# Optimization experiments

Measured on AMD Instinct MI355X. Metric: run time of the kernel, lower is better.

The kernel has to match this reference:

```python
import jax, jax.numpy as jnp
import numpy as np

B, T, C, H = 4, 2048, 768, 64

def setup_inputs() -> dict:
    key = jax.random.key(0)
    k1, k2, k3, k4 = jax.random.split(key, 4)
    x = jax.random.normal(k1, (B, T, C), dtype=jnp.float32)
    # Dense kernels (glorot-ish scale)
    s = 1.0 / np.sqrt(C)
    Wq = jax.random.normal(k2, (C, H), dtype=jnp.float32) * s
    Wk = jax.random.normal(k3, (C, H), dtype=jnp.float32) * s
    Wv = jax.random.normal(k4, (C, H), dtype=jnp.float32) * s
    return {"x": x, "Wq": Wq, "Wk": Wk, "Wv": Wv}

def reference(x, Wq, Wk, Wv):
    # q, k, v: [B, T, H]
    q = jnp.einsum('btc,ch->bth', x, Wq)
    k = jnp.einsum('btc,ch->bth', x, Wk)
    v = jnp.einsum('btc,ch->bth', x, Wv)
    scale = k.shape[-1] ** -0.5
    # scores: [B, T, T]
    scores = jnp.einsum('bth,bsh->bts', q, k) * scale
    # causal mask: lower-triangular allowed
    causal = jnp.tril(jnp.ones((T, T), dtype=bool))
    scores = jnp.where(causal, scores, -jnp.inf)
    weights = jax.nn.softmax(scores, axis=-1)
    # dropout is inactive at inference (Keras default training=False)
    out = jnp.einsum('bts,bsh->bth', weights, v)
    return out
```

## Files before the change

kernel.cpp:

```cpp
#include <hip/hip_runtime.h>
#include <hip/hip_bf16.h>
#include <math.h>

constexpr int BB = 4;
constexpr int TT = 2048;
constexpr int CC = 768;
constexpr int HH = 64;
constexpr int NSPLIT = 4;

typedef __attribute__((ext_vector_type(8))) short bf16x8;
typedef __attribute__((ext_vector_type(4))) float f32x4;

__device__ inline ushort f2bf(float f) {
    uint u = __float_as_uint(f);
    u += 0x7fffu + ((u >> 16) & 1u);
    return (ushort)(u >> 16);
}

__device__ inline bf16x8 cvt8(const float4 a, const float4 b) {
    union { bf16x8 v; __hip_bfloat162 h[4]; } u;
    u.h[0] = __float22bfloat162_rn(make_float2(a.x, a.y));
    u.h[1] = __float22bfloat162_rn(make_float2(a.z, a.w));
    u.h[2] = __float22bfloat162_rn(make_float2(b.x, b.y));
    u.h[3] = __float22bfloat162_rn(make_float2(b.z, b.w));
    return u.v;
}

__global__ __launch_bounds__(256) void prep_w(const float* __restrict__ Wq,
                                              const float* __restrict__ Wk,
                                              const float* __restrict__ Wv,
                                              ushort* __restrict__ Wt) {
    const int k0  = blockIdx.x * 64;
    const int mat = blockIdx.y;
    const float* W = (mat == 0) ? Wq : (mat == 1) ? Wk : Wv;
    __shared__ ushort tile[64 * 66];
    const int tid = threadIdx.x;

    for (int i = tid; i < 1024; i += 256) {
        int kk = i >> 4, c = i & 15;
        float4 f = ((const float4*)W)[(k0 + kk) * 16 + c];
        ushort* d = &tile[kk * 66 + c * 4];
        d[0] = f2bf(f.x); d[1] = f2bf(f.y); d[2] = f2bf(f.z); d[3] = f2bf(f.w);
    }
    __syncthreads();
    for (int i = tid; i < 512; i += 256) {
        int n = i >> 3, c8 = i & 7;
        bf16x8 v;
        #pragma unroll
        for (int j = 0; j < 8; ++j)
            ((ushort*)&v)[j] = tile[(c8 * 8 + j) * 66 + n];
        *(bf16x8*)&Wt[(size_t)(mat * 64 + n) * CC + k0 + c8 * 8] = v;
    }
}

__global__ __launch_bounds__(256) void qkv_mfma(const float* __restrict__ x,
                                                const ushort* __restrict__ Wt,
                                                ushort* __restrict__ qg,
                                                ushort* __restrict__ kg,
                                                ushort* __restrict__ vtg) {
    __shared__ ushort vts[64 * 24];
    const int tid  = threadIdx.x;
    const int row0 = blockIdx.x * 16;
    const int lane = tid & 63, w = tid >> 6;
    const int l15  = lane & 15, quad = lane >> 4;
    const int cg   = w * 48;

    f32x4 acc[3];
    #pragma unroll
    for (int i = 0; i < 3; ++i) acc[i] = (f32x4){0.f, 0.f, 0.f, 0.f};

    const float* xrow = x + (size_t)(row0 + l15) * CC;
    #pragma unroll 4
    for (int kc = 0; kc < 24; ++kc) {
        const float4* xp = (const float4*)(xrow + kc * 32) + quad * 2;
        bf16x8 a = cvt8(xp[0], xp[1]);
        #pragma unroll
        for (int nt = 0; nt < 3; ++nt) {
            bf16x8 bfr = *(const bf16x8*)
                &Wt[(size_t)(cg + nt * 16 + l15) * CC + kc * 32 + quad * 8];
            acc[nt] = __builtin_amdgcn_mfma_f32_16x16x32_bf16(a, bfr, acc[nt], 0, 0, 0);
        }
    }

    #pragma unroll
    for (int nt = 0; nt < 3; ++nt) {
        int n = cg + nt * 16 + l15;
        #pragma unroll
        for (int r = 0; r < 4; ++r) {
            int row = row0 + quad * 4 + r;
            float vacc = acc[nt][r];
            if (n < 64)       qg[(size_t)row * HH + n] = f2bf(vacc * 0.125f);
            else if (n < 128) kg[(size_t)row * HH + (n - 64)] = f2bf(vacc);
            else              vts[(n - 128) * 24 + (quad * 4 + r)] = f2bf(vacc);
        }
    }
    __syncthreads();
    if (tid < 128) {
        int h = tid >> 1, p = tid & 1;
        int b = row0 >> 11, tl = row0 & 2047;
        bf16x8 v = *(const bf16x8*)&vts[h * 24 + p * 8];
        *(bf16x8*)&vtg[(size_t)b * (HH * TT) + (size_t)h * TT + tl + p * 8] = v;
    }
}

__global__ __launch_bounds__(128) void attn_split(const ushort* __restrict__ qg,
                                                  const ushort* __restrict__ kg,
                                                  const ushort* __restrict__ vtg,
                                                  float* __restrict__ Op,
                                                  float* __restrict__ ml) {
    const int qt2 = blockIdx.x, b = blockIdx.y, split = blockIdx.z;
    const int tid  = threadIdx.x;
    const int lane = tid & 63, w = tid >> 6;
    const int l15  = lane & 15, quad = lane >> 4;
    const int t0   = qt2 * 32;
    const int pidx = ((b * 64 + qt2) << 2) + split;

    const int ntile = (qt2 >> 1) + 1;
    const int lo = (ntile * split) >> 2;
    const int hi = (ntile * (split + 1)) >> 2;

    if (lo >= hi) {
        float4 z = (float4){0.f, 0.f, 0.f, 0.f};
        float4* op4 = (float4*)(Op + (size_t)pidx * 2048);
        #pragma unroll
        for (int j = 0; j < 4; ++j) op4[tid * 4 + j] = z;
        if (tid < 32) {
            ml[pidx * 64 + tid]      = -1e30f;
            ml[pidx * 64 + 32 + tid] = 0.f;
        }
        return;
    }

    __shared__ ushort Ps[2][16 * 72];

    const ushort* qp = &qg[(size_t)(b * TT + t0 + w * 16 + l15) * HH + quad * 8];
    bf16x8 qa0 = *(const bf16x8*)qp;
    bf16x8 qa1 = *(const bf16x8*)(qp + 32);

    f32x4 po[4];
    #pragma unroll
    for (int i = 0; i < 4; ++i) po[i] = (f32x4){0.f, 0.f, 0.f, 0.f};
    float mrun[4] = {-1e30f, -1e30f, -1e30f, -1e30f};
    float lrun[4] = {0.f, 0.f, 0.f, 0.f};

    for (int st = lo; st < hi; ++st) {
        f32x4 sf[4];
        #pragma unroll
        for (int nt = 0; nt < 4; ++nt) {
            const ushort* kp =
                &kg[(size_t)(b * TT + st * 64 + nt * 16 + l15) * HH + quad * 8];
            bf16x8 b0 = *(const bf16x8*)kp;
            bf16x8 b1 = *(const bf16x8*)(kp + 32);
            f32x4 z = (f32x4){0.f, 0.f, 0.f, 0.f};
            z = __builtin_amdgcn_mfma_f32_16x16x32_bf16(qa0, b0, z, 0, 0, 0);
            sf[nt] = __builtin_amdgcn_mfma_f32_16x16x32_bf16(qa1, b1, z, 0, 0, 0);
        }

        float p[4][4];
        float rm[4] = {-1e30f, -1e30f, -1e30f, -1e30f};
        if (st == ntile - 1) {
            #pragma unroll
            for (int nt = 0; nt < 4; ++nt) {
                int s_abs = st * 64 + nt * 16 + l15;
                #pragma unroll
                for (int r = 0; r < 4; ++r) {
                    int t_abs = t0 + w * 16 + quad * 4 + r;
                    float v = (s_abs > t_abs) ? -1e30f : sf[nt][r];
                    p[nt][r] = v;
                    rm[r] = fmaxf(rm[r], v);
                }
            }
        } else {
            #pragma unroll
            for (int nt = 0; nt < 4; ++nt)
                #pragma unroll
                for (int r = 0; r < 4; ++r) {
                    p[nt][r] = sf[nt][r];
                    rm[r] = fmaxf(rm[r], sf[nt][r]);
                }
        }
        float alpha[4], rs[4] = {0.f, 0.f, 0.f, 0.f};
        #pragma unroll
        for (int r = 0; r < 4; ++r) {
            float v = rm[r];
            v = fmaxf(v, __shfl_xor(v, 1, 64));
            v = fmaxf(v, __shfl_xor(v, 2, 64));
            v = fmaxf(v, __shfl_xor(v, 4, 64));
            v = fmaxf(v, __shfl_xor(v, 8, 64));
            float mnew = fmaxf(mrun[r], v);
            alpha[r] = __expf(mrun[r] - mnew);
            mrun[r] = mnew;
        }
        #pragma unroll
        for (int nt = 0; nt < 4; ++nt)
            #pragma unroll
            for (int r = 0; r < 4; ++r) {
                float e = __expf(p[nt][r] - mrun[r]);
                p[nt][r] = e;
                rs[r] += e;
            }
        #pragma unroll
        for (int r = 0; r < 4; ++r) {
            float v = rs[r];
            v += __shfl_xor(v, 1, 64);
            v += __shfl_xor(v, 2, 64);
            v += __shfl_xor(v, 4, 64);
            v += __shfl_xor(v, 8, 64);
            lrun[r] = lrun[r] * alpha[r] + v;
        }
        #pragma unroll
        for (int jj = 0; jj < 4; ++jj)
            #pragma unroll
            for (int r = 0; r < 4; ++r)
                po[jj][r] *= alpha[r];

        #pragma unroll
        for (int nt = 0; nt < 4; ++nt)
            #pragma unroll
            for (int r = 0; r < 4; ++r)
                Ps[w][(quad * 4 + r) * 72 + nt * 16 + l15] = f2bf(p[nt][r]);
        bf16x8 pa0 = *(const bf16x8*)&Ps[w][l15 * 72 + quad * 8];
        bf16x8 pa1 = *(const bf16x8*)&Ps[w][l15 * 72 + 32 + quad * 8];

        #pragma unroll
        for (int jj = 0; jj < 4; ++jj) {
            const ushort* vp =
                &vtg[(size_t)b * (HH * TT) + (size_t)(jj * 16 + l15) * TT + st * 64 + quad * 8];
            bf16x8 b0 = *(const bf16x8*)vp;
            bf16x8 b1 = *(const bf16x8*)(vp + 32);
            po[jj] = __builtin_amdgcn_mfma_f32_16x16x32_bf16(pa0, b0, po[jj], 0, 0, 0);
            po[jj] = __builtin_amdgcn_mfma_f32_16x16x32_bf16(pa1, b1, po[jj], 0, 0, 0);
        }
    }

    #pragma unroll
    for (int jj = 0; jj < 4; ++jj)
        #pragma unroll
        for (int r = 0; r < 4; ++r)
            Op[(size_t)pidx * 2048 + (w * 16 + quad * 4 + r) * 64 + jj * 16 + l15] =
                po[jj][r];
    if (l15 == 0) {
        #pragma unroll
        for (int r = 0; r < 4; ++r) {
            int row = w * 16 + quad * 4 + r;
            ml[pidx * 64 + row]      = mrun[r];
            ml[pidx * 64 + 32 + row] = lrun[r];
        }
    }
}

__global__ __launch_bounds__(256) void attn_merge(const float* __restrict__ Op,
                                                  const float* __restrict__ ml,
                                                  float* __restrict__ out) {
    const int tid = threadIdx.x;
    const int w = tid >> 6, lane = tid & 63;
    const int row = blockIdx.x * 4 + w;
    const int b = row >> 11, t = row & 2047;
    const int qt2 = t >> 5, rl = t & 31;
    const int pbase = ((b * 64 + qt2) << 2);

    float m[NSPLIT], l[NSPLIT];
    #pragma unroll
    for (int i = 0; i < NSPLIT; ++i) {
        m[i] = ml[(pbase + i) * 64 + rl];
        l[i] = ml[(pbase + i) * 64 + 32 + rl];
    }
    float M = fmaxf(fmaxf(m[0], m[1]), fmaxf(m[2], m[3]));
    float wgt[NSPLIT], L = 0.f;
    #pragma unroll
    for (int i = 0; i < NSPLIT; ++i) {
        wgt[i] = __expf(m[i] - M);
        L += wgt[i] * l[i];
    }
    float acc = 0.f;
    #pragma unroll
    for (int i = 0; i < NSPLIT; ++i)
        acc += wgt[i] * Op[(size_t)(pbase + i) * 2048 + rl * 64 + lane];
    out[(size_t)row * HH + lane] = acc / L;
}

extern "C" void kernel_launch(void* const* d_in, const int* in_sizes, int n_in,
                              void* d_out, int out_size, void* d_ws, size_t ws_size,
                              hipStream_t stream)
{
    const float* x  = (const float*)d_in[0];
    const float* Wq = (const float*)d_in[1];
    const float* Wk = (const float*)d_in[2];
    const float* Wv = (const float*)d_in[3];
    float* out = (float*)d_out;

    ushort* qg  = (ushort*)d_ws;
    ushort* kg  = qg  + (size_t)BB * TT * HH;
    ushort* vtg = kg  + (size_t)BB * TT * HH;
    ushort* Wt  = vtg + (size_t)BB * TT * HH;
    float*  Op  = (float*)(Wt + (size_t)3 * HH * CC);
    float*  ml  = Op + (size_t)1024 * 2048;

    prep_w    <<<dim3(12, 3),           dim3(256), 0, stream>>>(Wq, Wk, Wv, Wt);
    qkv_mfma  <<<dim3((BB * TT) / 16),  dim3(256), 0, stream>>>(x, Wt, qg, kg, vtg);
    attn_split<<<dim3(64, BB, NSPLIT),  dim3(128), 0, stream>>>(qg, kg, vtg, Op, ml);
    attn_merge<<<dim3((BB * TT) / 4),   dim3(256), 0, stream>>>(Op, ml, out);
}
```

Before: 139.2 us.

## Prefetch K/V and x/W tiles into registers and raise split count to eight

The QKV projection kernel now keeps a four-deep register ring of x and weight fragments, so global loads are issued ahead of the MFMAs that consume them. The attention split kernel prefetches the next K tile and issues the V loads before the softmax step, hiding load latency behind compute. The KV split count doubles from four to eight, which raises parallelism across the grid. In exchange it doubles the partial-output workspace and merge traffic, launches more empty blocks for short rows, and increases register pressure.

```diff
diff --git a/kernel.cpp b/kernel.cpp
--- a/kernel.cpp
+++ b/kernel.cpp
@@ -6,7 +6,7 @@
 constexpr int TT = 2048;
 constexpr int CC = 768;
 constexpr int HH = 64;
-constexpr int NSPLIT = 4;
+constexpr int NSPLIT = 8;
 
 typedef __attribute__((ext_vector_type(8))) short bf16x8;
 typedef __attribute__((ext_vector_type(4))) float f32x4;
@@ -69,17 +69,38 @@
     #pragma unroll
     for (int i = 0; i < 3; ++i) acc[i] = (f32x4){0.f, 0.f, 0.f, 0.f};
 
-    const float* xrow = x + (size_t)(row0 + l15) * CC;
-    #pragma unroll 4
+    const float*  xrow  = x + (size_t)(row0 + l15) * CC;
+    const ushort* wbase = Wt + (size_t)(cg + l15) * CC + quad * 8;
+
+    float4 xb[4][2];
+    bf16x8 wb[4][3];
+    #pragma unroll
+    for (int i = 0; i < 4; ++i) {
+        const float4* xp = (const float4*)(xrow + i * 32) + quad * 2;
+        xb[i][0] = xp[0];
+        xb[i][1] = xp[1];
+        #pragma unroll
+        for (int nt = 0; nt < 3; ++nt)
+            wb[i][nt] = *(const bf16x8*)(wbase + (size_t)nt * 16 * CC + i * 32);
+    }
+
+    #pragma unroll
     for (int kc = 0; kc < 24; ++kc) {
-        const float4* xp = (const float4*)(xrow + kc * 32) + quad * 2;
-        bf16x8 a = cvt8(xp[0], xp[1]);
-        #pragma unroll
-        for (int nt = 0; nt < 3; ++nt) {
-            bf16x8 bfr = *(const bf16x8*)
-                &Wt[(size_t)(cg + nt * 16 + l15) * CC + kc * 32 + quad * 8];
-            acc[nt] = __builtin_amdgcn_mfma_f32_16x16x32_bf16(a, bfr, acc[nt], 0, 0, 0);
-        }
+        const int cur = kc & 3;
+        bf16x8 a  = cvt8(xb[cur][0], xb[cur][1]);
+        bf16x8 w0 = wb[cur][0], w1 = wb[cur][1], w2 = wb[cur][2];
+        const int nx = kc + 4;
+        if (nx < 24) {
+            const float4* xp = (const float4*)(xrow + nx * 32) + quad * 2;
+            xb[cur][0] = xp[0];
+            xb[cur][1] = xp[1];
+            #pragma unroll
+            for (int nt = 0; nt < 3; ++nt)
+                wb[cur][nt] = *(const bf16x8*)(wbase + (size_t)nt * 16 * CC + nx * 32);
+        }
+        acc[0] = __builtin_amdgcn_mfma_f32_16x16x32_bf16(a, w0, acc[0], 0, 0, 0);
+        acc[1] = __builtin_amdgcn_mfma_f32_16x16x32_bf16(a, w1, acc[1], 0, 0, 0);
+        acc[2] = __builtin_amdgcn_mfma_f32_16x16x32_bf16(a, w2, acc[2], 0, 0, 0);
     }
 
     #pragma unroll
@@ -113,11 +134,11 @@
     const int lane = tid & 63, w = tid >> 6;
     const int l15  = lane & 15, quad = lane >> 4;
     const int t0   = qt2 * 32;
-    const int pidx = ((b * 64 + qt2) << 2) + split;
+    const int pidx = ((b * 64 + qt2) << 3) + split;
 
     const int ntile = (qt2 >> 1) + 1;
-    const int lo = (ntile * split) >> 2;
-    const int hi = (ntile * (split + 1)) >> 2;
+    const int lo = (ntile * split) >> 3;
+    const int hi = (ntile * (split + 1)) >> 3;
 
     if (lo >= hi) {
         float4 z = (float4){0.f, 0.f, 0.f, 0.f};
@@ -137,23 +158,44 @@
     bf16x8 qa0 = *(const bf16x8*)qp;
     bf16x8 qa1 = *(const bf16x8*)(qp + 32);
 
+    const ushort* kbb = &kg[(size_t)(b * TT + l15) * HH + quad * 8];
+    const ushort* vbb = &vtg[(size_t)b * (HH * TT) + (size_t)l15 * TT + quad * 8];
+
     f32x4 po[4];
     #pragma unroll
     for (int i = 0; i < 4; ++i) po[i] = (f32x4){0.f, 0.f, 0.f, 0.f};
     float mrun[4] = {-1e30f, -1e30f, -1e30f, -1e30f};
     float lrun[4] = {0.f, 0.f, 0.f, 0.f};
 
+    bf16x8 kb[8], vb[8];
+    #pragma unroll
+    for (int nt = 0; nt < 4; ++nt) {
+        const ushort* kp = kbb + (size_t)(lo * 64 + nt * 16) * HH;
+        kb[2 * nt]     = *(const bf16x8*)kp;
+        kb[2 * nt + 1] = *(const bf16x8*)(kp + 32);
+    }
+
     for (int st = lo; st < hi; ++st) {
         f32x4 sf[4];
         #pragma unroll
         for (int nt = 0; nt < 4; ++nt) {
-            const ushort* kp =
-                &kg[(size_t)(b * TT + st * 64 + nt * 16 + l15) * HH + quad * 8];
-            bf16x8 b0 = *(const bf16x8*)kp;
-            bf16x8 b1 = *(const bf16x8*)(kp + 32);
             f32x4 z = (f32x4){0.f, 0.f, 0.f, 0.f};
-            z = __builtin_amdgcn_mfma_f32_16x16x32_bf16(qa0, b0, z, 0, 0, 0);
-            sf[nt] = __builtin_amdgcn_mfma_f32_16x16x32_bf16(qa1, b1, z, 0, 0, 0);
+            z = __builtin_amdgcn_mfma_f32_16x16x32_bf16(qa0, kb[2 * nt], z, 0, 0, 0);
+            sf[nt] = __builtin_amdgcn_mfma_f32_16x16x32_bf16(qa1, kb[2 * nt + 1], z, 0, 0, 0);
+        }
+        if (st + 1 < hi) {
+            #pragma unroll
+            for (int nt = 0; nt < 4; ++nt) {
+                const ushort* kp = kbb + (size_t)((st + 1) * 64 + nt * 16) * HH;
+                kb[2 * nt]     = *(const bf16x8*)kp;
+                kb[2 * nt + 1] = *(const bf16x8*)(kp + 32);
+            }
+        }
+        #pragma unroll
+        for (int jj = 0; jj < 4; ++jj) {
+            const ushort* vp = vbb + (size_t)(jj * 16) * TT + st * 64;
+            vb[2 * jj]     = *(const bf16x8*)vp;
+            vb[2 * jj + 1] = *(const bf16x8*)(vp + 32);
         }
 
         float p[4][4];
@@ -224,12 +266,8 @@
 
         #pragma unroll
         for (int jj = 0; jj < 4; ++jj) {
-            const ushort* vp =
-                &vtg[(size_t)b * (HH * TT) + (size_t)(jj * 16 + l15) * TT + st * 64 + quad * 8];
-            bf16x8 b0 = *(const bf16x8*)vp;
-            bf16x8 b1 = *(const bf16x8*)(vp + 32);
-            po[jj] = __builtin_amdgcn_mfma_f32_16x16x32_bf16(pa0, b0, po[jj], 0, 0, 0);
-            po[jj] = __builtin_amdgcn_mfma_f32_16x16x32_bf16(pa1, b1, po[jj], 0, 0, 0);
+            po[jj] = __builtin_amdgcn_mfma_f32_16x16x32_bf16(pa0, vb[2 * jj], po[jj], 0, 0, 0);
+            po[jj] = __builtin_amdgcn_mfma_f32_16x16x32_bf16(pa1, vb[2 * jj + 1], po[jj], 0, 0, 0);
         }
     }
 
@@ -257,7 +295,7 @@
     const int row = blockIdx.x * 4 + w;
     const int b = row >> 11, t = row & 2047;
     const int qt2 = t >> 5, rl = t & 31;
-    const int pbase = ((b * 64 + qt2) << 2);
+    const int pbase = ((b * 64 + qt2) << 3);
 
     float m[NSPLIT], l[NSPLIT];
     #pragma unroll
@@ -265,7 +303,9 @@
         m[i] = ml[(pbase + i) * 64 + rl];
         l[i] = ml[(pbase + i) * 64 + 32 + rl];
     }
-    float M = fmaxf(fmaxf(m[0], m[1]), fmaxf(m[2], m[3]));
+    float M = -1e30f;
+    #pragma unroll
+    for (int i = 0; i < NSPLIT; ++i) M = fmaxf(M, m[i]);
     float wgt[NSPLIT], L = 0.f;
     #pragma unroll
     for (int i = 0; i < NSPLIT; ++i) {
@@ -294,7 +334,7 @@
     ushort* vtg = kg  + (size_t)BB * TT * HH;
     ushort* Wt  = vtg + (size_t)BB * TT * HH;
     float*  Op  = (float*)(Wt + (size_t)3 * HH * CC);
-    float*  ml  = Op + (size_t)1024 * 2048;
+    float*  ml  = Op + (size_t)2048 * 2048;
 
     prep_w    <<<dim3(12, 3),           dim3(256), 0, stream>>>(Wq, Wk, Wv, Wt);
     qkv_mfma  <<<dim3((BB * TT) / 16),  dim3(256), 0, stream>>>(x, Wt, qg, kg, vtg);
```

Result: faster. 134.7 us (-3.2%).
